# Optimization experiments

Measured on AMD Instinct MI355X. Metric: run time of the kernel, lower is better.

The kernel has to match this reference:

```python
import jax, jax.numpy as jnp
import numpy as np

N_NODES = 100000
N_EDGES = 1600000
D = 128
RESIDUAL_WEIGHT = 0.001


def setup_inputs() -> dict:
    key = jax.random.key(0)
    k = jax.random.split(key, 7)
    x = jax.random.normal(k[0], (N_NODES, D), dtype=jnp.float32)
    edge_index = jax.random.randint(k[1], (2, N_EDGES), 0, N_NODES, dtype=jnp.int32)
    s = 1.0 / np.sqrt(D)
    Wl = jax.random.normal(k[2], (D, D), dtype=jnp.float32) * s
    bl = jax.random.normal(k[3], (D,), dtype=jnp.float32) * s
    Wr = jax.random.normal(k[4], (D, D), dtype=jnp.float32) * s
    Wres = jax.random.normal(k[5], (D, D), dtype=jnp.float32) * s
    bres = jax.random.normal(k[6], (D,), dtype=jnp.float32) * s
    return {"x": x, "edge_index": edge_index, "Wl": Wl, "bl": bl,
            "Wr": Wr, "Wres": Wres, "bres": bres}


def reference(x, edge_index, Wl, bl, Wr, Wres, bres):
    # PyG SAGEConv(aggr='sum'): messages x_j flow src -> dst
    src, dst = edge_index[0], edge_index[1]
    agg = jax.ops.segment_sum(x[src], dst, num_segments=x.shape[0])  # [N, D]
    # lin_l(agg) (with bias) + lin_r(x) (root weight, no bias)
    h_sage = agg @ Wl.T + bl + x @ Wr.T
    # residual Linear
    h_res = x @ Wres.T + bres
    rw = jnp.float32(RESIDUAL_WEIGHT)
    # dropout p=0 (eval) -> identity
    return rw * h_sage + (1.0 - rw) * h_res
```

## Files before the change

### kernel.cpp

```cpp
#include <hip/hip_runtime.h>
#include <hip/hip_bf16.h>
#include <stdint.h>

#define DD 128
#define RW 0.001f
#define CHUNK 4096
#define CAP 4096
#define YS 8.0f

#if defined(__has_builtin)
#if __has_builtin(__builtin_amdgcn_cvt_scalef32_pk_fp4_f32) && __has_builtin(__builtin_amdgcn_cvt_scalef32_pk_f32_fp4)
#define HAVE_FP4 1
#endif
#endif
#ifndef HAVE_FP4
#define HAVE_FP4 0
#endif

#if HAVE_FP4
#define XBB 64
#else
#define XBB 128
#endif

typedef __attribute__((ext_vector_type(4))) float f32x4;
typedef __attribute__((ext_vector_type(2))) float f32x2;
typedef __attribute__((ext_vector_type(8))) short bf16x8;

static __device__ __forceinline__ uint32_t pack2(float lo, float hi){
  return __builtin_amdgcn_perm(__float_as_uint(hi), __float_as_uint(lo), 0x07060302u);
}

static __device__ __forceinline__ ushort rne_bf16(float f){
  uint32_t u = __float_as_uint(f);
  return (ushort)((u + 0x7fffu + ((u >> 16) & 1u)) >> 16);
}

__global__ __launch_bounds__(512) void fused_prep(
    const int* __restrict__ src, const int* __restrict__ dst,
    int* __restrict__ gcnt, uint32_t* __restrict__ recs, int E, int nb, int nchunk,
    const float* __restrict__ x, uint8_t* __restrict__ xb, int n8, int nq, int M,
    const float* __restrict__ Wl, const float* __restrict__ bl,
    const float* __restrict__ Wr, const float* __restrict__ Wres,
    const float* __restrict__ bres, ushort* __restrict__ Wfb, float* __restrict__ bc)
{
  __shared__ uint32_t srec[CHUNK];
  __shared__ uint16_t sb[CHUNK];
  __shared__ int hcnt[800];
  __shared__ int hbase[800];
  __shared__ int lcur[800];
  int t = threadIdx.x;
  int b = blockIdx.x;

  if (b < nchunk){
    int base = b * CHUNK;
    for (int i = t; i < nb; i += 512){ hcnt[i] = 0; lcur[i] = 0; }
    __syncthreads();
    #pragma unroll
    for (int k = 0; k < 8; k++){
      int idx = k * 512 + t;
      int e = base + idx;
      uint16_t bb = 0xFFFFu;
      if (e < E){
        int d = dst[e];
        bb = (uint16_t)(d >> 7);
        srec[idx] = ((uint32_t)(d & 127) << 17) | (uint32_t)src[e];
        atomicAdd(&hcnt[bb], 1);
      }
      sb[idx] = bb;
    }
    __syncthreads();
    for (int i = t; i < nb; i += 512)
      hbase[i] = hcnt[i] ? atomicAdd(&gcnt[i], hcnt[i]) : 0;
    __syncthreads();
    #pragma unroll
    for (int k = 0; k < 8; k++){
      int idx = k * 512 + t;
      uint16_t bb = sb[idx];
      if (bb != 0xFFFFu){
        int p = hbase[bb] + atomicAdd(&lcur[bb], 1);
        if (p < CAP) recs[(size_t)bb * CAP + p] = srec[idx];
      }
    }
  } else if (b < nchunk + nq){
    int i = (b - nchunk) * 512 + t;
    if (i < n8){
      const f32x4* p = (const f32x4*)(x + (size_t)i * 8);
      f32x4 f0 = p[0], f1 = p[1];
#if HAVE_FP4
      uint32_t d = 0;
      d = __builtin_amdgcn_cvt_scalef32_pk_fp4_f32(d, f0[0], f0[1], 1.0f, 0);
      d = __builtin_amdgcn_cvt_scalef32_pk_fp4_f32(d, f0[2], f0[3], 1.0f, 1);
      d = __builtin_amdgcn_cvt_scalef32_pk_fp4_f32(d, f1[0], f1[1], 1.0f, 2);
      d = __builtin_amdgcn_cvt_scalef32_pk_fp4_f32(d, f1[2], f1[3], 1.0f, 3);
      *(uint32_t*)(xb + (size_t)i * 4) = d;
#else
      int pk0 = __builtin_amdgcn_cvt_pk_fp8_f32(f0[0], f0[1], 0, false);
      pk0     = __builtin_amdgcn_cvt_pk_fp8_f32(f0[2], f0[3], pk0, true);
      int pk1 = __builtin_amdgcn_cvt_pk_fp8_f32(f1[0], f1[1], 0, false);
      pk1     = __builtin_amdgcn_cvt_pk_fp8_f32(f1[2], f1[3], pk1, true);
      uint2 w; w.x = (uint32_t)pk0; w.y = (uint32_t)pk1;
      *(uint2*)(xb + (size_t)i * 8) = w;
#endif
    }
  } else {
    int i = (b - nchunk - nq) * 512 + t;
    if (i < 8 && i * 16 < XBB){
      uint4 z = {0u, 0u, 0u, 0u};
      *(uint4*)(xb + (size_t)M * XBB + i * 16) = z;
    }
    if (i < DD * 256){
      int c = i >> 8, k = i & 255;
      float v;
      if (k < DD) v = RW * Wr[c * DD + k] + (1.f - RW) * Wres[c * DD + k];
      else        v = (RW / YS) * Wl[c * DD + (k - DD)];
      Wfb[i] = rne_bf16(v);
      if (i < DD) bc[i] = RW * bl[i] + (1.f - RW) * bres[i];
    }
  }
}

__global__ __launch_bounds__(512) void bsort(uint32_t* __restrict__ recs,
                                             const int* __restrict__ gcnt,
                                             int2* __restrict__ meta, int M){
  __shared__ uint32_t srec[CAP];
  __shared__ uint32_t ssorted[CAP];
  __shared__ int h[128], pstart[128], lc[128];
  int t = threadIdx.x;
  int b = blockIdx.x;
  int s = b * CAP;
  int cnt = gcnt[b];
  if (cnt > CAP) cnt = CAP;

  if (t < 128){ h[t] = 0; lc[t] = 0; }
  __syncthreads();
  for (int i = t; i < cnt; i += 512){
    uint32_t r = recs[s + i];
    srec[i] = r;
    atomicAdd(&h[(r >> 17) & 127u], 1);
  }
  __syncthreads();
  int val = (t < 128) ? h[t] : 0;
  #pragma unroll
  for (int off = 1; off < 128; off <<= 1){
    if (t < 128) pstart[t] = val;
    __syncthreads();
    if (t < 128 && t >= off) val += pstart[t - off];
    __syncthreads();
  }
  if (t < 128){
    pstart[t] = val - h[t];
    int node = b * 128 + t;
    if (node < M) meta[node] = make_int2(s + pstart[t], h[t]);
  }
  __syncthreads();
  for (int i = t; i < cnt; i += 512){
    uint32_t r = srec[i];
    int n7 = (int)((r >> 17) & 127u);
    int pos = pstart[n7] + atomicAdd(&lc[n7], 1);
    ssorted[pos] = r & 0x1FFFFu;
  }
  __syncthreads();
  for (int i = t; i < cnt; i += 512)
    recs[s + i] = ssorted[i];
}

__global__ __launch_bounds__(256, 4) void agg(const uint8_t* __restrict__ xb,
                                              const uint32_t* __restrict__ csr,
                                              const int2* __restrict__ meta,
                                              uint8_t* __restrict__ ybar, int N)
{
  int wid = (int)((blockIdx.x * 256 + threadIdx.x) >> 6);
  if (wid >= N) return;
  int lane = threadIdx.x & 63;
  int2 mc = meta[wid];
  int start = mc.x, cnt = mc.y;
  uint32_t raw = csr[start + lane];
  uint32_t vidx = (lane < cnt) ? raw : (uint32_t)N;

#if HAVE_FP4
  int voff = lane;
#else
  int voff = lane * 2;
#endif

  f32x2 acc0 = (f32x2){0.f,0.f}, acc1 = (f32x2){0.f,0.f};
  f32x2 acc2 = (f32x2){0.f,0.f}, acc3 = (f32x2){0.f,0.f};

  int n64 = cnt < 64 ? cnt : 64;
  int nit = (n64 + 15) >> 4;
  for (int it = 0; it < nit; it++){
    int bb = it << 4;
    int vbuf[16];
    #pragma unroll
    for (int k = 0; k < 16; k++){
      uint32_t s = (uint32_t)__builtin_amdgcn_readlane((int)vidx, bb + k);
#if HAVE_FP4
      vbuf[k] = *(const uint8_t*)(xb + (size_t)s * XBB + voff);
#else
      vbuf[k] = *(const ushort*)(xb + (size_t)s * XBB + voff);
#endif
    }
    #pragma unroll
    for (int k = 0; k < 16; k++){
#if HAVE_FP4
      f32x2 f = __builtin_amdgcn_cvt_scalef32_pk_f32_fp4(vbuf[k], 1.0f, 0);
#else
      f32x2 f = __builtin_amdgcn_cvt_pk_f32_fp8(vbuf[k], false);
#endif
      if ((k & 3) == 0) acc0 += f;
      else if ((k & 3) == 1) acc1 += f;
      else if ((k & 3) == 2) acc2 += f;
      else acc3 += f;
    }
  }
  for (int j = 64; j < cnt; j++){
    uint32_t s = csr[start + j];
#if HAVE_FP4
    int v = *(const uint8_t*)(xb + (size_t)s * XBB + voff);
    f32x2 f = __builtin_amdgcn_cvt_scalef32_pk_f32_fp4(v, 1.0f, 0);
#else
    int v = *(const ushort*)(xb + (size_t)s * XBB + voff);
    f32x2 f = __builtin_amdgcn_cvt_pk_f32_fp8(v, false);
#endif
    acc0 += f;
  }

  f32x2 r = (acc0 + acc1) + (acc2 + acc3);
  float a0 = r[0] * YS, a1 = r[1] * YS;
  int pk = __builtin_amdgcn_cvt_pk_fp8_f32(a0, a1, 0, false);
  *(ushort*)(ybar + (size_t)wid * DD + lane * 2) = (ushort)(pk & 0xFFFF);
}

__global__ __launch_bounds__(512, 4) void gemm2(
    const float* __restrict__ x, const uint8_t* __restrict__ ybar,
    const ushort* __restrict__ Wfb, const float* __restrict__ bc,
    float* __restrict__ out, int M)
{
  __shared__ char sX[32768];
  int tid = threadIdx.x;
  int lane = tid & 63, w = tid >> 6;
  int wr = w >> 2, wcol = w & 3;
  int l15 = lane & 15, lhi = lane >> 4;
  int rowbase = blockIdx.x * 128 + wr * 64;
  int colbase = wcol * 32;

  f32x4 acc[4][2];
  #pragma unroll
  for (int a = 0; a < 4; a++)
    #pragma unroll
    for (int b = 0; b < 2; b++) acc[a][b] = (f32x4){0.f,0.f,0.f,0.f};

  #pragma unroll
  for (int p = 0; p < 4; p++){
    int g   = p * 512 + tid;
    int row = g >> 4;
    int cx  = tid & 15;
    int grow = blockIdx.x * 128 + row;
    if (grow >= M) grow = M - 1;
    const float* ap = x + (size_t)grow * DD + cx * 8;
    f32x4 f0 = *(const f32x4*)ap;
    f32x4 f1 = *(const f32x4*)(ap + 4);
    uint4 wv;
    wv.x = pack2(f0[0], f0[1]);
    wv.y = pack2(f0[2], f0[3]);
    wv.z = pack2(f1[0], f1[1]);
    wv.w = pack2(f1[2], f1[3]);
    int sw = (row << 8) | ((cx * 16) ^ ((row & 7) << 4));
    *(uint4*)&sX[sw] = wv;
  }
  __syncthreads();

  #pragma unroll
  for (int ks = 0; ks < 4; ks++){
    bf16x8 afr[4];
    #pragma unroll
    for (int rt = 0; rt < 4; rt++){
      int row = wr * 64 + rt * 16 + l15;
      int byte = (row << 8) | ((ks * 64 + lhi * 16) ^ ((row & 7) << 4));
      afr[rt] = *(const bf16x8*)&sX[byte];
    }
    #pragma unroll
    for (int ct = 0; ct < 2; ct++){
      int colm = colbase + ct * 16 + l15;
      bf16x8 bfr = *(const bf16x8*)(Wfb + (size_t)colm * 256 + ks * 32 + lhi * 8);
      #pragma unroll
      for (int rt = 0; rt < 4; rt++)
        acc[rt][ct] = __builtin_amdgcn_mfma_f32_16x16x32_bf16(bfr, afr[rt], acc[rt][ct], 0, 0, 0);
    }
  }
  __syncthreads();

  #pragma unroll
  for (int p = 0; p < 4; p++){
    int g   = p * 512 + tid;
    int row = g >> 4;
    int cx  = tid & 15;
    int grow = blockIdx.x * 128 + row;
    if (grow >= M) grow = M - 1;
    uint2 rv = *(const uint2*)(ybar + (size_t)grow * DD + cx * 8);
    f32x2 e0 = __builtin_amdgcn_cvt_pk_f32_fp8((int)rv.x, false);
    f32x2 e1 = __builtin_amdgcn_cvt_pk_f32_fp8((int)rv.x, true);
    f32x2 e2 = __builtin_amdgcn_cvt_pk_f32_fp8((int)rv.y, false);
    f32x2 e3 = __builtin_amdgcn_cvt_pk_f32_fp8((int)rv.y, true);
    uint4 wv;
    wv.x = pack2(e0[0], e0[1]);
    wv.y = pack2(e1[0], e1[1]);
    wv.z = pack2(e2[0], e2[1]);
    wv.w = pack2(e3[0], e3[1]);
    int sw = (row << 8) | ((cx * 16) ^ ((row & 7) << 4));
    *(uint4*)&sX[sw] = wv;
  }
  __syncthreads();

  #pragma unroll
  for (int ks = 0; ks < 4; ks++){
    bf16x8 afr[4];
    #pragma unroll
    for (int rt = 0; rt < 4; rt++){
      int row = wr * 64 + rt * 16 + l15;
      int byte = (row << 8) | ((ks * 64 + lhi * 16) ^ ((row & 7) << 4));
      afr[rt] = *(const bf16x8*)&sX[byte];
    }
    #pragma unroll
    for (int ct = 0; ct < 2; ct++){
      int colm = colbase + ct * 16 + l15;
      bf16x8 bfr = *(const bf16x8*)(Wfb + (size_t)colm * 256 + 128 + ks * 32 + lhi * 8);
      #pragma unroll
      for (int rt = 0; rt < 4; rt++)
        acc[rt][ct] = __builtin_amdgcn_mfma_f32_16x16x32_bf16(bfr, afr[rt], acc[rt][ct], 0, 0, 0);
    }
  }

  #pragma unroll
  for (int ct = 0; ct < 2; ct++){
    int col = colbase + ct * 16 + lhi * 4;
    f32x4 b4 = *(const f32x4*)&bc[col];
    #pragma unroll
    for (int rt = 0; rt < 4; rt++){
      int row = rowbase + rt * 16 + l15;
      if (row < M){
        f32x4 o = acc[rt][ct] + b4;
        *(f32x4*)(out + (size_t)row * DD + col) = o;
      }
    }
  }
}

extern "C" void kernel_launch(void* const* d_in, const int* in_sizes, int n_in,
                              void* d_out, int out_size, void* d_ws, size_t ws_size,
                              hipStream_t stream) {
  const float* x    = (const float*)d_in[0];
  const int*   ei   = (const int*)d_in[1];
  const float* Wl   = (const float*)d_in[2];
  const float* bl   = (const float*)d_in[3];
  const float* Wr   = (const float*)d_in[4];
  const float* Wres = (const float*)d_in[5];
  const float* bres = (const float*)d_in[6];
  float* out = (float*)d_out;

  int M = in_sizes[0] / DD;
  int E = in_sizes[1] / 2;
  const int* esrc = ei;
  const int* edst = ei + E;
  int nb = (M + 127) >> 7;

  char* wsp = (char*)d_ws;
  size_t off = 0;
  uint8_t*  xb   = (uint8_t*) (wsp + off); off += (size_t)(M + 1) * 128; off = (off + 255) & ~255ull;
  uint8_t*  ybar = (uint8_t*) (wsp + off); off += (size_t)M * DD;        off = (off + 255) & ~255ull;
  uint32_t* recs = (uint32_t*)(wsp + off); off += (size_t)800 * CAP * 4;
  ushort*   Wfb  = (ushort*)  (wsp + off); off += DD * 256 * 2;
  float*    bc   = (float*)   (wsp + off); off += 512;
  int*      gcnt = (int*)     (wsp + off); off += sizeof(int) * 1024;
  int2*     meta = (int2*)    (wsp + off); off += sizeof(int2) * (size_t)M;

  int n8 = M * 16;
  int nchunk = (E + CHUNK - 1) / CHUNK;
  int nq = (n8 + 511) / 512;
  int nprep = (DD * 256 + 511) / 512;

  hipMemsetAsync(gcnt, 0, sizeof(int) * 1024, stream);
  fused_prep<<<nchunk + nq + nprep, 512, 0, stream>>>(
      esrc, edst, gcnt, recs, E, nb, nchunk,
      x, xb, n8, nq, M,
      Wl, bl, Wr, Wres, bres, Wfb, bc);
  bsort<<<nb, 512, 0, stream>>>(recs, gcnt, meta, M);
  agg<<<((size_t)M * 64 + 255) / 256, 256, 0, stream>>>(xb, recs, meta, ybar, M);
  gemm2<<<(M + 127) / 128, 512, 0, stream>>>(x, ybar, Wfb, bc, out, M);
}
```

Baseline: 110.5 us.

## Overlap x-half GEMM with aggregation in one launch, then add ybar half separately

Splits the GEMM into an x-dependent half and a ybar-dependent half. The x half (with bias) now runs in the same launch as the neighbor aggregation, using separate blocks, so that tensor-core work overlaps the gather-bound aggregation. A second kernel computes the ybar half and read-modify-writes the output. This adds an extra read and write of the fp32 output and a fourth launch stays, so the overlap has to outweigh that extra traffic.

New measurement: 134.7 us. 21.9% more time.

```diff
diff --git a/kernel.cpp b/kernel.cpp
--- a/kernel.cpp
+++ b/kernel.cpp
@@ -165,81 +165,76 @@
     recs[s + i] = ssorted[i];
 }
 
-__global__ __launch_bounds__(256, 4) void agg(const uint8_t* __restrict__ xb,
-                                              const uint32_t* __restrict__ csr,
-                                              const int2* __restrict__ meta,
-                                              uint8_t* __restrict__ ybar, int N)
-{
-  int wid = (int)((blockIdx.x * 256 + threadIdx.x) >> 6);
-  if (wid >= N) return;
-  int lane = threadIdx.x & 63;
-  int2 mc = meta[wid];
-  int start = mc.x, cnt = mc.y;
-  uint32_t raw = csr[start + lane];
-  uint32_t vidx = (lane < cnt) ? raw : (uint32_t)N;
-
-#if HAVE_FP4
-  int voff = lane;
-#else
-  int voff = lane * 2;
-#endif
-
-  f32x2 acc0 = (f32x2){0.f,0.f}, acc1 = (f32x2){0.f,0.f};
-  f32x2 acc2 = (f32x2){0.f,0.f}, acc3 = (f32x2){0.f,0.f};
-
-  int n64 = cnt < 64 ? cnt : 64;
-  int nit = (n64 + 15) >> 4;
-  for (int it = 0; it < nit; it++){
-    int bb = it << 4;
-    int vbuf[16];
-    #pragma unroll
-    for (int k = 0; k < 16; k++){
-      uint32_t s = (uint32_t)__builtin_amdgcn_readlane((int)vidx, bb + k);
-#if HAVE_FP4
-      vbuf[k] = *(const uint8_t*)(xb + (size_t)s * XBB + voff);
-#else
-      vbuf[k] = *(const ushort*)(xb + (size_t)s * XBB + voff);
-#endif
-    }
-    #pragma unroll
-    for (int k = 0; k < 16; k++){
-#if HAVE_FP4
-      f32x2 f = __builtin_amdgcn_cvt_scalef32_pk_f32_fp4(vbuf[k], 1.0f, 0);
-#else
-      f32x2 f = __builtin_amdgcn_cvt_pk_f32_fp8(vbuf[k], false);
-#endif
-      if ((k & 3) == 0) acc0 += f;
-      else if ((k & 3) == 1) acc1 += f;
-      else if ((k & 3) == 2) acc2 += f;
-      else acc3 += f;
-    }
-  }
-  for (int j = 64; j < cnt; j++){
-    uint32_t s = csr[start + j];
-#if HAVE_FP4
-    int v = *(const uint8_t*)(xb + (size_t)s * XBB + voff);
-    f32x2 f = __builtin_amdgcn_cvt_scalef32_pk_f32_fp4(v, 1.0f, 0);
-#else
-    int v = *(const ushort*)(xb + (size_t)s * XBB + voff);
-    f32x2 f = __builtin_amdgcn_cvt_pk_f32_fp8(v, false);
-#endif
-    acc0 += f;
-  }
-
-  f32x2 r = (acc0 + acc1) + (acc2 + acc3);
-  float a0 = r[0] * YS, a1 = r[1] * YS;
-  int pk = __builtin_amdgcn_cvt_pk_fp8_f32(a0, a1, 0, false);
-  *(ushort*)(ybar + (size_t)wid * DD + lane * 2) = (ushort)(pk & 0xFFFF);
-}
-
-__global__ __launch_bounds__(512, 4) void gemm2(
-    const float* __restrict__ x, const uint8_t* __restrict__ ybar,
+__global__ __launch_bounds__(512, 4) void agg_gemmA(
+    const float* __restrict__ x, const uint8_t* __restrict__ xb,
+    const uint32_t* __restrict__ csr, const int2* __restrict__ meta,
     const ushort* __restrict__ Wfb, const float* __restrict__ bc,
-    float* __restrict__ out, int M)
+    uint8_t* __restrict__ ybar, float* __restrict__ out, int M, int nbA)
 {
   __shared__ char sX[32768];
   int tid = threadIdx.x;
   int lane = tid & 63, w = tid >> 6;
+
+  if ((int)blockIdx.x >= nbA){
+    int wid = ((int)blockIdx.x - nbA) * 8 + w;
+    if (wid >= M) return;
+    int2 mc = meta[wid];
+    int start = mc.x, cnt = mc.y;
+    uint32_t raw = csr[start + lane];
+    uint32_t vidx = (lane < cnt) ? raw : (uint32_t)M;
+
+#if HAVE_FP4
+    int voff = lane;
+#else
+    int voff = lane * 2;
+#endif
+    f32x2 acc0 = (f32x2){0.f,0.f}, acc1 = (f32x2){0.f,0.f};
+    f32x2 acc2 = (f32x2){0.f,0.f}, acc3 = (f32x2){0.f,0.f};
+
+    int n64 = cnt < 64 ? cnt : 64;
+    int nit = (n64 + 15) >> 4;
+    for (int it = 0; it < nit; it++){
+      int bb = it << 4;
+      int vbuf[16];
+      #pragma unroll
+      for (int k = 0; k < 16; k++){
+        uint32_t s = (uint32_t)__builtin_amdgcn_readlane((int)vidx, bb + k);
+#if HAVE_FP4
+        vbuf[k] = *(const uint8_t*)(xb + (size_t)s * XBB + voff);
+#else
+        vbuf[k] = *(const ushort*)(xb + (size_t)s * XBB + voff);
+#endif
+      }
+      #pragma unroll
+      for (int k = 0; k < 16; k++){
+#if HAVE_FP4
+        f32x2 f = __builtin_amdgcn_cvt_scalef32_pk_f32_fp4(vbuf[k], 1.0f, 0);
+#else
+        f32x2 f = __builtin_amdgcn_cvt_pk_f32_fp8(vbuf[k], false);
+#endif
+        if ((k & 3) == 0) acc0 += f;
+        else if ((k & 3) == 1) acc1 += f;
+        else if ((k & 3) == 2) acc2 += f;
+        else acc3 += f;
+      }
+    }
+    for (int j = 64; j < cnt; j++){
+      uint32_t s = csr[start + j];
+#if HAVE_FP4
+      int v = *(const uint8_t*)(xb + (size_t)s * XBB + voff);
+      f32x2 f = __builtin_amdgcn_cvt_scalef32_pk_f32_fp4(v, 1.0f, 0);
+#else
+      int v = *(const ushort*)(xb + (size_t)s * XBB + voff);
+      f32x2 f = __builtin_amdgcn_cvt_pk_f32_fp8(v, false);
+#endif
+      acc0 += f;
+    }
+    f32x2 r = (acc0 + acc1) + (acc2 + acc3);
+    int pk = __builtin_amdgcn_cvt_pk_fp8_f32(r[0] * YS, r[1] * YS, 0, false);
+    *(ushort*)(ybar + (size_t)wid * DD + lane * 2) = (ushort)(pk & 0xFFFF);
+    return;
+  }
+
   int wr = w >> 2, wcol = w & 3;
   int l15 = lane & 15, lhi = lane >> 4;
   int rowbase = blockIdx.x * 128 + wr * 64;
@@ -289,7 +284,39 @@
         acc[rt][ct] = __builtin_amdgcn_mfma_f32_16x16x32_bf16(bfr, afr[rt], acc[rt][ct], 0, 0, 0);
     }
   }
-  __syncthreads();
+
+  #pragma unroll
+  for (int ct = 0; ct < 2; ct++){
+    int col = colbase + ct * 16 + lhi * 4;
+    f32x4 b4 = *(const f32x4*)&bc[col];
+    #pragma unroll
+    for (int rt = 0; rt < 4; rt++){
+      int row = rowbase + rt * 16 + l15;
+      if (row < M){
+        f32x4 o = acc[rt][ct] + b4;
+        *(f32x4*)(out + (size_t)row * DD + col) = o;
+      }
+    }
+  }
+}
+
+__global__ __launch_bounds__(512, 4) void gemmB(
+    const uint8_t* __restrict__ ybar, const ushort* __restrict__ Wfb,
+    float* __restrict__ out, int M)
+{
+  __shared__ char sX[32768];
+  int tid = threadIdx.x;
+  int lane = tid & 63, w = tid >> 6;
+  int wr = w >> 2, wcol = w & 3;
+  int l15 = lane & 15, lhi = lane >> 4;
+  int rowbase = blockIdx.x * 128 + wr * 64;
+  int colbase = wcol * 32;
+
+  f32x4 acc[4][2];
+  #pragma unroll
+  for (int a = 0; a < 4; a++)
+    #pragma unroll
+    for (int b = 0; b < 2; b++) acc[a][b] = (f32x4){0.f,0.f,0.f,0.f};
 
   #pragma unroll
   for (int p = 0; p < 4; p++){
@@ -335,13 +362,14 @@
   #pragma unroll
   for (int ct = 0; ct < 2; ct++){
     int col = colbase + ct * 16 + lhi * 4;
-    f32x4 b4 = *(const f32x4*)&bc[col];
     #pragma unroll
     for (int rt = 0; rt < 4; rt++){
       int row = rowbase + rt * 16 + l15;
       if (row < M){
-        f32x4 o = acc[rt][ct] + b4;
-        *(f32x4*)(out + (size_t)row * DD + col) = o;
+        float* op = out + (size_t)row * DD + col;
+        f32x4 o = *(f32x4*)op;
+        o += acc[rt][ct];
+        *(f32x4*)op = o;
       }
     }
   }
@@ -386,6 +414,7 @@
       x, xb, n8, nq, M,
       Wl, bl, Wr, Wres, bres, Wfb, bc);
   bsort<<<nb, 512, 0, stream>>>(recs, gcnt, meta, M);
-  agg<<<((size_t)M * 64 + 255) / 256, 256, 0, stream>>>(xb, recs, meta, ybar, M);
-  gemm2<<<(M + 127) / 128, 512, 0, stream>>>(x, ybar, Wfb, bc, out, M);
-}
+  int naggblk = (M + 7) / 8;
+  agg_gemmA<<<nb + naggblk, 512, 0, stream>>>(x, xb, recs, meta, Wfb, bc, ybar, out, M, nb);
+  gemmB<<<nb, 512, 0, stream>>>(ybar, Wfb, out, M);
+}
```
